# Performance work log

Hardware: AMD Instinct MI355X
Metric: run time of the kernel (lower is better)

The kernel has to match this reference:

```python
import jax, jax.numpy as jnp
import numpy as np

N = 50000   # total nodes
E = 600000  # total edges
F = 128     # in_features == hidden_features
H = 128
L = 4       # layers_count
B = 256     # number of graphs in batch
M = 200     # molecule_features
OUT = 12    # out_features
MH = H // 4 # molecular head width


def setup_inputs() -> dict:
    key = jax.random.key(0)
    ks = jax.random.split(key, 16)
    x = jax.random.normal(ks[0], (N, F), dtype=jnp.float32)
    edge_index = jax.random.randint(ks[1], (2, E), 0, N, dtype=jnp.int64)
    # sorted segment ids; guarantee every graph has >=1 node
    batch = jnp.sort(jnp.concatenate([
        jnp.arange(B, dtype=jnp.int64),
        jax.random.randint(ks[2], (N - B,), 0, B, dtype=jnp.int64)]))
    molecule_features = jax.random.normal(ks[3], (B, M), dtype=jnp.float32)
    s = 0.05
    Ws = jax.random.normal(ks[4], (L, H, H), dtype=jnp.float32) * s
    bs = jnp.zeros((L, H), dtype=jnp.float32)
    Wm = jax.random.normal(ks[5], (M, MH), dtype=jnp.float32) * s
    bm = jnp.zeros((MH,), dtype=jnp.float32)
    gamma = jnp.ones((MH,), dtype=jnp.float32)   # BatchNorm1d affine (eval mode, running stats 0/1)
    beta = jnp.zeros((MH,), dtype=jnp.float32)
    W1 = jax.random.normal(ks[6], (2 * H + MH, H), dtype=jnp.float32) * s  # mlp in = 288
    b1 = jnp.zeros((H,), dtype=jnp.float32)
    W2 = jax.random.normal(ks[7], (H, OUT), dtype=jnp.float32) * s
    b2 = jnp.zeros((OUT,), dtype=jnp.float32)
    return dict(x=x, edge_index=edge_index, batch=batch,
                molecule_features=molecule_features, Ws=Ws, bs=bs,
                Wm=Wm, bm=bm, gamma=gamma, beta=beta,
                W1=W1, b1=b1, W2=W2, b2=b2)


def gcn_conv(x, src, dst, W, b):
    # GCNConv: D^{-1/2} (A + I) D^{-1/2} X W + b, degrees include self loops
    ones = jnp.ones((E,), dtype=x.dtype)
    deg = jax.ops.segment_sum(ones, dst, num_segments=N) + 1.0  # self loop
    dis = jax.lax.rsqrt(deg)
    norm = dis[src] * dis[dst]                      # [E]
    xw = x @ W                                      # [N,H]
    msg = xw[src] * norm[:, None]                   # gather + scale
    agg = jax.ops.segment_sum(msg, dst, num_segments=N)
    agg = agg + xw * (dis * dis)[:, None]           # self-loop term
    return agg + b


def reference(x, edge_index, batch, molecule_features, Ws, bs, Wm, bm,
              gamma, beta, W1, b1, W2, b2):
    src, dst = edge_index[0], edge_index[1]
    h = x
    for l in range(L):
        y = jax.nn.relu(gcn_conv(h, src, dst, Ws[l], bs[l]))
        h = y + h  # residual (in == hidden); dropout is identity in eval
    max_pool = jax.ops.segment_max(h, batch, num_segments=B)
    add_pool = jax.ops.segment_sum(h, batch, num_segments=B)
    # molecular head: Linear -> Dropout(eval=identity) -> BatchNorm1d(eval) -> ReLU
    mol = molecule_features @ Wm + bm
    mol = jax.nn.relu(mol * gamma + beta)  # running_mean=0, running_var=1
    z = jnp.concatenate((max_pool, add_pool, mol), axis=1)  # [B, 288]
    z = jax.nn.relu(z @ W1 + b1)
    return z @ W2 + b2  # [B, OUT]
```

## Files before the change

### kernel.cpp

```cpp
#include <hip/hip_runtime.h>
#include <hip/hip_fp16.h>
#include <math.h>

static constexpr int NN  = 50000;
static constexpr int NE  = 600000;
static constexpr int HD  = 128;
static constexpr int NL  = 4;
static constexpr int NB  = 256;
static constexpr int NM  = 200;
static constexpr int NO  = 12;
static constexpr int NMH = 32;

#define MAX4(ac, b) { (ac).x = fmaxf((ac).x,(b).x); (ac).y = fmaxf((ac).y,(b).y); (ac).z = fmaxf((ac).z,(b).z); (ac).w = fmaxf((ac).w,(b).w); }
#define ADD4(ac, b) { (ac).x += (b).x; (ac).y += (b).y; (ac).z += (b).z; (ac).w += (b).w; }

typedef short bfx8 __attribute__((ext_vector_type(8)));
typedef float f32x4 __attribute__((ext_vector_type(4)));

__device__ __forceinline__ unsigned short f2bf(float f) {
  unsigned int u = __float_as_uint(f);
  unsigned int r = (u + 0x7fffu + ((u >> 16) & 1u)) >> 16;
  return (unsigned short)r;
}
__device__ __forceinline__ float bflo(unsigned int p) { return __uint_as_float(p << 16); }
__device__ __forceinline__ float bfhi(unsigned int p) { return __uint_as_float(p & 0xffff0000u); }
__device__ __forceinline__ float h2f_hi(unsigned e) {
  return __half2float(__ushort_as_half((unsigned short)(e >> 16)));
}

__global__ void k_hist(const int* __restrict__ dst, int* __restrict__ counts) {
  int e = blockIdx.x * blockDim.x + threadIdx.x;
  if (e < NE) atomicAdd(&counts[dst[e]], 1);
}

__global__ void k_scan1(const int* __restrict__ counts, int* __restrict__ incl,
                        int* __restrict__ bsum, float* __restrict__ dis) {
  __shared__ int s[256];
  int i = blockIdx.x * 256 + threadIdx.x;
  int v = (i < NN) ? counts[i] : 0;
  if (i < NN) dis[i] = rsqrtf((float)(v + 1));
  s[threadIdx.x] = v;
  __syncthreads();
  for (int off = 1; off < 256; off <<= 1) {
    int t = (threadIdx.x >= off) ? s[threadIdx.x - off] : 0;
    __syncthreads();
    s[threadIdx.x] += t;
    __syncthreads();
  }
  if (i < NN) incl[i] = s[threadIdx.x];
  if (threadIdx.x == 255) bsum[blockIdx.x] = s[255];
}

__global__ void k_scan2(const int* __restrict__ bsum, int* __restrict__ boff, int nblocks) {
  __shared__ int s[256];
  int v = (threadIdx.x < nblocks) ? bsum[threadIdx.x] : 0;
  s[threadIdx.x] = v;
  __syncthreads();
  for (int off = 1; off < 256; off <<= 1) {
    int t = (threadIdx.x >= off) ? s[threadIdx.x - off] : 0;
    __syncthreads();
    s[threadIdx.x] += t;
    __syncthreads();
  }
  boff[threadIdx.x] = s[threadIdx.x] - v;
}

__global__ void k_scan3(const int* __restrict__ counts, int* __restrict__ rowst, const int* __restrict__ boff) {
  int i = blockIdx.x * 256 + threadIdx.x;
  if (i < NN) {
    rowst[i] = rowst[i] - counts[i] + boff[blockIdx.x];
    if (i == NN - 1) rowst[NN] = NE;
  }
}

__global__ void k_fill(const int* __restrict__ src, const int* __restrict__ dst,
                       const int* __restrict__ rowst, const float* __restrict__ dis,
                       int* __restrict__ cur, unsigned* __restrict__ csr) {
  int e = blockIdx.x * blockDim.x + threadIdx.x;
  if (e < NE) {
    int d = dst[e];
    int s = src[e];
    int p = atomicAdd(&cur[d], 1);
    unsigned hb = (unsigned)__half_as_ushort(__float2half(dis[s]));
    csr[rowst[d] + p] = (hb << 16) | (unsigned)s;
  }
}

__global__ void k_goffs(const int* __restrict__ batch, int* __restrict__ goffs) {
  int i = blockIdx.x * blockDim.x + threadIdx.x;
  if (i >= NN) return;
  int b = batch[i];
  if (i == 0) {
    for (int g = 0; g <= b; ++g) goffs[g] = 0;
  } else {
    int pb = batch[i - 1];
    for (int g = pb + 1; g <= b; ++g) goffs[g] = i;
  }
  if (i == NN - 1) goffs[NB] = NN;
}

__global__ void k_tobf(const float4* __restrict__ in, ushort4* __restrict__ outb, int n4) {
  int i = blockIdx.x * blockDim.x + threadIdx.x;
  if (i < n4) {
    float4 v = in[i];
    outb[i] = make_ushort4(f2bf(v.x), f2bf(v.y), f2bf(v.z), f2bf(v.w));
  }
}

__global__ void k_wT(const float* __restrict__ Ws, unsigned short* __restrict__ wT) {
  int i = blockIdx.x * blockDim.x + threadIdx.x;
  if (i < NL * HD * HD) {
    int l = i >> 14, rem = i & 16383, n = rem >> 7, k = rem & 127;
    wT[i] = f2bf(Ws[l * 16384 + k * 128 + n]);
  }
}

__launch_bounds__(256)
__global__ void k_gemm_mfma(const unsigned short* __restrict__ A,
                            const unsigned short* __restrict__ WT,
                            unsigned short* __restrict__ C) {
  const int wave = threadIdx.x >> 6;
  const int lane = threadIdx.x & 63;
  const int m_base = blockIdx.x * 128 + wave * 32;
  const int lr = lane & 15;
  const int kg = lane >> 4;

  f32x4 acc[2][8];
#pragma unroll
  for (int mi = 0; mi < 2; ++mi)
#pragma unroll
    for (int nj = 0; nj < 8; ++nj) acc[mi][nj] = (f32x4){0.f, 0.f, 0.f, 0.f};

  int ra0 = m_base + lr;       if (ra0 > NN - 1) ra0 = NN - 1;
  int ra1 = m_base + 16 + lr;  if (ra1 > NN - 1) ra1 = NN - 1;

#pragma unroll
  for (int kb = 0; kb < 4; ++kb) {
    const int k0 = kb * 32 + kg * 8;
    bfx8 a0 = *(const bfx8*)&A[(size_t)ra0 * HD + k0];
    bfx8 a1 = *(const bfx8*)&A[(size_t)ra1 * HD + k0];
#pragma unroll
    for (int nj = 0; nj < 8; ++nj) {
      bfx8 b = *(const bfx8*)&WT[(nj * 16 + lr) * HD + k0];
      acc[0][nj] = __builtin_amdgcn_mfma_f32_16x16x32_bf16(a0, b, acc[0][nj], 0, 0, 0);
      acc[1][nj] = __builtin_amdgcn_mfma_f32_16x16x32_bf16(a1, b, acc[1][nj], 0, 0, 0);
    }
  }

  const int col = lane & 15;
  const int rbase = (lane >> 4) * 4;
#pragma unroll
  for (int mi = 0; mi < 2; ++mi) {
#pragma unroll
    for (int r = 0; r < 4; ++r) {
      int row = m_base + mi * 16 + rbase + r;
      if (row < NN) {
#pragma unroll
        for (int nj = 0; nj < 8; ++nj) {
          C[(size_t)row * HD + nj * 16 + col] = f2bf(acc[mi][nj][r]);
        }
      }
    }
  }
}

#define AGG_EDGE(e, p) { float nm = h2f_hi(e) * dn; \
    acc.x += nm * bflo((p).x); acc.y += nm * bfhi((p).x); \
    acc.z += nm * bflo((p).y); acc.w += nm * bfhi((p).y); }

__launch_bounds__(256)
__global__ void k_agg_h(const unsigned short* __restrict__ xw, const float* __restrict__ dis,
                        const int* __restrict__ rowst, const unsigned* __restrict__ csr,
                        const float* __restrict__ bias, const unsigned short* __restrict__ hinb,
                        unsigned short* __restrict__ houtb, int fh) {
  int slot = threadIdx.x >> 4;
  int lane = threadIdx.x & 15;
  int n = blockIdx.x * 16 + slot;
  if (n >= NN) return;

  const uint2* xwb = (const uint2*)xw;
  const int fo = fh * 16 + lane;

  float dn = dis[n];
  float4 acc;
  {
    uint2 p = xwb[(size_t)n * 32 + fo];
    float sl = dn * dn;
    acc.x = bflo(p.x) * sl; acc.y = bfhi(p.x) * sl;
    acc.z = bflo(p.y) * sl; acc.w = bfhi(p.y) * sl;
  }

  int s0 = rowst[n], s1 = rowst[n + 1];
  int idx = s0;
  for (; idx + 8 <= s1; idx += 8) {
    unsigned e0 = csr[idx],     e1 = csr[idx + 1], e2 = csr[idx + 2], e3 = csr[idx + 3];
    unsigned e4 = csr[idx + 4], e5 = csr[idx + 5], e6 = csr[idx + 6], e7 = csr[idx + 7];
    uint2 p0 = xwb[(size_t)(e0 & 0xffffu) * 32 + fo];
    uint2 p1 = xwb[(size_t)(e1 & 0xffffu) * 32 + fo];
    uint2 p2 = xwb[(size_t)(e2 & 0xffffu) * 32 + fo];
    uint2 p3 = xwb[(size_t)(e3 & 0xffffu) * 32 + fo];
    uint2 p4 = xwb[(size_t)(e4 & 0xffffu) * 32 + fo];
    uint2 p5 = xwb[(size_t)(e5 & 0xffffu) * 32 + fo];
    uint2 p6 = xwb[(size_t)(e6 & 0xffffu) * 32 + fo];
    uint2 p7 = xwb[(size_t)(e7 & 0xffffu) * 32 + fo];
    AGG_EDGE(e0, p0); AGG_EDGE(e1, p1); AGG_EDGE(e2, p2); AGG_EDGE(e3, p3);
    AGG_EDGE(e4, p4); AGG_EDGE(e5, p5); AGG_EDGE(e6, p6); AGG_EDGE(e7, p7);
  }
  for (; idx + 4 <= s1; idx += 4) {
    unsigned e0 = csr[idx], e1 = csr[idx + 1], e2 = csr[idx + 2], e3 = csr[idx + 3];
    uint2 p0 = xwb[(size_t)(e0 & 0xffffu) * 32 + fo];
    uint2 p1 = xwb[(size_t)(e1 & 0xffffu) * 32 + fo];
    uint2 p2 = xwb[(size_t)(e2 & 0xffffu) * 32 + fo];
    uint2 p3 = xwb[(size_t)(e3 & 0xffffu) * 32 + fo];
    AGG_EDGE(e0, p0); AGG_EDGE(e1, p1); AGG_EDGE(e2, p2); AGG_EDGE(e3, p3);
  }
  for (; idx < s1; ++idx) {
    unsigned e0 = csr[idx];
    uint2 p0 = xwb[(size_t)(e0 & 0xffffu) * 32 + fo];
    AGG_EDGE(e0, p0);
  }

  float4 b4 = *(const float4*)&bias[fh * 64 + lane * 4];
  uint2 hp = ((const uint2*)hinb)[(size_t)n * 32 + fo];
  float4 outv;
  outv.x = fmaxf(acc.x + b4.x, 0.f) + bflo(hp.x);
  outv.y = fmaxf(acc.y + b4.y, 0.f) + bfhi(hp.x);
  outv.z = fmaxf(acc.z + b4.z, 0.f) + bflo(hp.y);
  outv.w = fmaxf(acc.w + b4.w, 0.f) + bfhi(hp.y);
  ((ushort4*)houtb)[(size_t)n * 32 + fo] =
      make_ushort4(f2bf(outv.x), f2bf(outv.y), f2bf(outv.z), f2bf(outv.w));
}

__launch_bounds__(1024)
__global__ void k_pool(const unsigned short* __restrict__ hb, const int* __restrict__ goffs,
                       float* __restrict__ pooled) {
  __shared__ float4 smax[32][32];
  __shared__ float4 ssum[32][32];
  int g = blockIdx.x;
  int slot = threadIdx.x >> 5;
  int lane = threadIdx.x & 31;
  int a = goffs[g], bnd = goffs[g + 1];
  const uint2* hb2 = (const uint2*)hb;

  float4 mx = make_float4(-INFINITY, -INFINITY, -INFINITY, -INFINITY);
  float4 sm = make_float4(0.f, 0.f, 0.f, 0.f);
  for (int i = a + slot; i < bnd; i += 32) {
    uint2 p = hb2[(size_t)i * 32 + lane];
    float4 v = make_float4(bflo(p.x), bfhi(p.x), bflo(p.y), bfhi(p.y));
    MAX4(mx, v);
    ADD4(sm, v);
  }
  smax[slot][lane] = mx;
  ssum[slot][lane] = sm;
  __syncthreads();
#pragma unroll
  for (int off = 16; off >= 1; off >>= 1) {
    if (slot < off) {
      float4 m2 = smax[slot + off][lane];
      float4 s2 = ssum[slot + off][lane];
      float4 m1 = smax[slot][lane];
      float4 s1 = ssum[slot][lane];
      MAX4(m1, m2);
      ADD4(s1, s2);
      smax[slot][lane] = m1;
      ssum[slot][lane] = s1;
    }
    __syncthreads();
  }
  if (slot == 0) {
    *(float4*)&pooled[g * 256 + lane * 4]       = smax[0][lane];
    *(float4*)&pooled[g * 256 + 128 + lane * 4] = ssum[0][lane];
  }
}

__global__ void k_head(const float* __restrict__ pooled, const float* __restrict__ mf,
                       const float* __restrict__ Wm, const float* __restrict__ bm,
                       const float* __restrict__ gamma, const float* __restrict__ beta,
                       const float* __restrict__ W1, const float* __restrict__ b1,
                       const float* __restrict__ W2, const float* __restrict__ b2,
                       float* __restrict__ out) {
  __shared__ float z[288];
  __shared__ float z1[128];
  int g = blockIdx.x, t = threadIdx.x;
  z[t] = pooled[g * 256 + t];
  z[128 + t] = pooled[g * 256 + 128 + t];
  if (t < NMH) {
    float acc = bm[t];
    for (int k = 0; k < NM; ++k) acc += mf[g * NM + k] * Wm[k * NMH + t];
    acc = acc * gamma[t] + beta[t];
    z[256 + t] = fmaxf(acc, 0.f);
  }
  __syncthreads();
  float acc = b1[t];
  for (int k = 0; k < 288; ++k) acc += z[k] * W1[k * HD + t];
  z1[t] = fmaxf(acc, 0.f);
  __syncthreads();
  if (t < NO) {
    float a2 = b2[t];
    for (int k = 0; k < HD; ++k) a2 += z1[k] * W2[k * NO + t];
    out[g * NO + t] = a2;
  }
}

extern "C" void kernel_launch(void* const* d_in, const int* in_sizes, int n_in,
                              void* d_out, int out_size, void* d_ws, size_t ws_size,
                              hipStream_t stream) {
  const float* x     = (const float*)d_in[0];
  const int*   eidx  = (const int*)d_in[1];
  const int*   batch = (const int*)d_in[2];
  const float* mf    = (const float*)d_in[3];
  const float* Ws    = (const float*)d_in[4];
  const float* bs    = (const float*)d_in[5];
  const float* Wm    = (const float*)d_in[6];
  const float* bm    = (const float*)d_in[7];
  const float* gamma = (const float*)d_in[8];
  const float* beta  = (const float*)d_in[9];
  const float* W1    = (const float*)d_in[10];
  const float* b1    = (const float*)d_in[11];
  const float* W2    = (const float*)d_in[12];
  const float* b2    = (const float*)d_in[13];
  float* out = (float*)d_out;

  const int* src = eidx;
  const int* dst = eidx + NE;

  char* w = (char*)d_ws;
  size_t off = 0;
  auto alloc = [&](size_t bytes) -> void* {
    void* p = w + off;
    off += (bytes + 255) & ~(size_t)255;
    return p;
  };
  float* dis    = (float*)alloc((size_t)NN * 4);
  unsigned short* xw  = (unsigned short*)alloc((size_t)NN * HD * 2);
  unsigned short* xbf = (unsigned short*)alloc((size_t)NN * HD * 2);
  unsigned short* hbf = (unsigned short*)alloc((size_t)NN * HD * 2);
  unsigned short* wT  = (unsigned short*)alloc((size_t)NL * HD * HD * 2);
  int* counts   = (int*)alloc((size_t)NN * 4);
  int* cur      = (int*)alloc((size_t)NN * 4);
  int* rowst    = (int*)alloc((size_t)(NN + 1) * 4);
  unsigned* csr = (unsigned*)alloc((size_t)NE * 4);
  int* bsum     = (int*)alloc(256 * 4);
  int* boff     = (int*)alloc(256 * 4);
  int* goffs    = (int*)alloc((size_t)(NB + 1) * 4);
  float* pooled = (float*)alloc((size_t)NB * 256 * 4);
  (void)ws_size;

  const int SB = (NN + 255) / 256;

  hipMemsetAsync(counts, 0, (size_t)NN * 4, stream);
  hipMemsetAsync(cur, 0, (size_t)NN * 4, stream);

  k_hist<<<(NE + 255) / 256, 256, 0, stream>>>(dst, counts);
  k_scan1<<<SB, 256, 0, stream>>>(counts, rowst, bsum, dis);
  k_scan2<<<1, 256, 0, stream>>>(bsum, boff, SB);
  k_scan3<<<SB, 256, 0, stream>>>(counts, rowst, boff);
  k_fill<<<(NE + 255) / 256, 256, 0, stream>>>(src, dst, rowst, dis, cur, csr);

  k_goffs<<<SB, 256, 0, stream>>>(batch, goffs);
  k_tobf<<<((NN * HD / 4) + 255) / 256, 256, 0, stream>>>((const float4*)x, (ushort4*)xbf, NN * HD / 4);
  k_wT<<<(NL * HD * HD + 255) / 256, 256, 0, stream>>>(Ws, wT);

  const int AB = (NN + 15) / 16;
  for (int l = 0; l < NL; ++l) {
    const unsigned short* gin_bf = (l == 0) ? xbf : hbf;
    k_gemm_mfma<<<(NN + 127) / 128, 256, 0, stream>>>(gin_bf, wT + (size_t)l * HD * HD, xw);
    k_agg_h<<<AB, 256, 0, stream>>>(xw, dis, rowst, csr, bs + (size_t)l * HD, gin_bf, hbf, 0);
    k_agg_h<<<AB, 256, 0, stream>>>(xw, dis, rowst, csr, bs + (size_t)l * HD, gin_bf, hbf, 1);
  }

  k_pool<<<NB, 1024, 0, stream>>>(hbf, goffs, pooled);
  k_head<<<NB, 128, 0, stream>>>(pooled, mf, Wm, bm, gamma, beta, W1, b1, W2, b2, out);
}
```

Baseline: 302.7 us.

## Merge feature-half aggregation passes into one wide-load kernel and fuse setup kernels

The two per-layer aggregation launches, each covering one half of the features, become a single kernel. In it every lane gathers 16 bytes (8 bf16 features) per neighbour, so the CSR row is walked once instead of twice per layer. The bf16 conversion, weight transpose and graph-offset kernels are folded into one setup launch. The CSR fill now decrements the histogram counts instead of using a separate zeroed cursor array, which drops one memset and one buffer. In exchange, each thread holds more accumulator registers, and edge order within a row changes, which can slightly alter the float summation order.

```diff
diff --git a/kernel.cpp b/kernel.cpp
--- a/kernel.cpp
+++ b/kernel.cpp
@@ -75,43 +75,42 @@
 
 __global__ void k_fill(const int* __restrict__ src, const int* __restrict__ dst,
                        const int* __restrict__ rowst, const float* __restrict__ dis,
-                       int* __restrict__ cur, unsigned* __restrict__ csr) {
+                       int* __restrict__ counts, unsigned* __restrict__ csr) {
   int e = blockIdx.x * blockDim.x + threadIdx.x;
   if (e < NE) {
     int d = dst[e];
     int s = src[e];
-    int p = atomicAdd(&cur[d], 1);
+    int o = atomicSub(&counts[d], 1);
     unsigned hb = (unsigned)__half_as_ushort(__float2half(dis[s]));
-    csr[rowst[d] + p] = (hb << 16) | (unsigned)s;
-  }
-}
-
-__global__ void k_goffs(const int* __restrict__ batch, int* __restrict__ goffs) {
+    csr[rowst[d] + o - 1] = (hb << 16) | (unsigned)s;
+  }
+}
+
+static constexpr int NT_TOBF = NN * HD / 4;
+static constexpr int NT_WT   = NL * HD * HD;
+static constexpr int NT_ALL  = NT_TOBF + NT_WT + NN;
+
+__global__ void k_setup(const float4* __restrict__ x4, ushort4* __restrict__ xbf4,
+                        const float* __restrict__ Ws, unsigned short* __restrict__ wT,
+                        const int* __restrict__ batch, int* __restrict__ goffs) {
   int i = blockIdx.x * blockDim.x + threadIdx.x;
-  if (i >= NN) return;
-  int b = batch[i];
-  if (i == 0) {
-    for (int g = 0; g <= b; ++g) goffs[g] = 0;
-  } else {
-    int pb = batch[i - 1];
-    for (int g = pb + 1; g <= b; ++g) goffs[g] = i;
-  }
-  if (i == NN - 1) goffs[NB] = NN;
-}
-
-__global__ void k_tobf(const float4* __restrict__ in, ushort4* __restrict__ outb, int n4) {
-  int i = blockIdx.x * blockDim.x + threadIdx.x;
-  if (i < n4) {
-    float4 v = in[i];
-    outb[i] = make_ushort4(f2bf(v.x), f2bf(v.y), f2bf(v.z), f2bf(v.w));
-  }
-}
-
-__global__ void k_wT(const float* __restrict__ Ws, unsigned short* __restrict__ wT) {
-  int i = blockIdx.x * blockDim.x + threadIdx.x;
-  if (i < NL * HD * HD) {
-    int l = i >> 14, rem = i & 16383, n = rem >> 7, k = rem & 127;
-    wT[i] = f2bf(Ws[l * 16384 + k * 128 + n]);
+  if (i < NT_TOBF) {
+    float4 v = x4[i];
+    xbf4[i] = make_ushort4(f2bf(v.x), f2bf(v.y), f2bf(v.z), f2bf(v.w));
+  } else if (i < NT_TOBF + NT_WT) {
+    int j = i - NT_TOBF;
+    int l = j >> 14, rem = j & 16383, n = rem >> 7, k = rem & 127;
+    wT[j] = f2bf(Ws[l * 16384 + k * 128 + n]);
+  } else if (i < NT_ALL) {
+    int j = i - NT_TOBF - NT_WT;
+    int b = batch[j];
+    if (j == 0) {
+      for (int g = 0; g <= b; ++g) goffs[g] = 0;
+    } else {
+      int pb = batch[j - 1];
+      for (int g = pb + 1; g <= b; ++g) goffs[g] = j;
+    }
+    if (j == NN - 1) goffs[NB] = NN;
   }
 }
 
@@ -164,30 +163,33 @@
   }
 }
 
-#define AGG_EDGE(e, p) { float nm = h2f_hi(e) * dn; \
-    acc.x += nm * bflo((p).x); acc.y += nm * bfhi((p).x); \
-    acc.z += nm * bflo((p).y); acc.w += nm * bfhi((p).y); }
+#define AGGE(e, p) { float nm = h2f_hi(e) * dn; \
+    acc[0] += nm * bflo((p).x); acc[1] += nm * bfhi((p).x); \
+    acc[2] += nm * bflo((p).y); acc[3] += nm * bfhi((p).y); \
+    acc[4] += nm * bflo((p).z); acc[5] += nm * bfhi((p).z); \
+    acc[6] += nm * bflo((p).w); acc[7] += nm * bfhi((p).w); }
 
 __launch_bounds__(256)
-__global__ void k_agg_h(const unsigned short* __restrict__ xw, const float* __restrict__ dis,
+__global__ void k_agg16(const unsigned short* __restrict__ xw, const float* __restrict__ dis,
                         const int* __restrict__ rowst, const unsigned* __restrict__ csr,
                         const float* __restrict__ bias, const unsigned short* __restrict__ hinb,
-                        unsigned short* __restrict__ houtb, int fh) {
+                        unsigned short* __restrict__ houtb) {
   int slot = threadIdx.x >> 4;
   int lane = threadIdx.x & 15;
   int n = blockIdx.x * 16 + slot;
   if (n >= NN) return;
 
-  const uint2* xwb = (const uint2*)xw;
-  const int fo = fh * 16 + lane;
+  const uint4* xw4 = (const uint4*)xw;
 
   float dn = dis[n];
-  float4 acc;
+  float acc[8];
   {
-    uint2 p = xwb[(size_t)n * 32 + fo];
+    uint4 p = xw4[(size_t)n * 16 + lane];
     float sl = dn * dn;
-    acc.x = bflo(p.x) * sl; acc.y = bfhi(p.x) * sl;
-    acc.z = bflo(p.y) * sl; acc.w = bfhi(p.y) * sl;
+    acc[0] = bflo(p.x) * sl; acc[1] = bfhi(p.x) * sl;
+    acc[2] = bflo(p.y) * sl; acc[3] = bfhi(p.y) * sl;
+    acc[4] = bflo(p.z) * sl; acc[5] = bfhi(p.z) * sl;
+    acc[6] = bflo(p.w) * sl; acc[7] = bfhi(p.w) * sl;
   }
 
   int s0 = rowst[n], s1 = rowst[n + 1];
@@ -195,40 +197,48 @@
   for (; idx + 8 <= s1; idx += 8) {
     unsigned e0 = csr[idx],     e1 = csr[idx + 1], e2 = csr[idx + 2], e3 = csr[idx + 3];
     unsigned e4 = csr[idx + 4], e5 = csr[idx + 5], e6 = csr[idx + 6], e7 = csr[idx + 7];
-    uint2 p0 = xwb[(size_t)(e0 & 0xffffu) * 32 + fo];
-    uint2 p1 = xwb[(size_t)(e1 & 0xffffu) * 32 + fo];
-    uint2 p2 = xwb[(size_t)(e2 & 0xffffu) * 32 + fo];
-    uint2 p3 = xwb[(size_t)(e3 & 0xffffu) * 32 + fo];
-    uint2 p4 = xwb[(size_t)(e4 & 0xffffu) * 32 + fo];
-    uint2 p5 = xwb[(size_t)(e5 & 0xffffu) * 32 + fo];
-    uint2 p6 = xwb[(size_t)(e6 & 0xffffu) * 32 + fo];
-    uint2 p7 = xwb[(size_t)(e7 & 0xffffu) * 32 + fo];
-    AGG_EDGE(e0, p0); AGG_EDGE(e1, p1); AGG_EDGE(e2, p2); AGG_EDGE(e3, p3);
-    AGG_EDGE(e4, p4); AGG_EDGE(e5, p5); AGG_EDGE(e6, p6); AGG_EDGE(e7, p7);
+    uint4 p0 = xw4[(size_t)(e0 & 0xffffu) * 16 + lane];
+    uint4 p1 = xw4[(size_t)(e1 & 0xffffu) * 16 + lane];
+    uint4 p2 = xw4[(size_t)(e2 & 0xffffu) * 16 + lane];
+    uint4 p3 = xw4[(size_t)(e3 & 0xffffu) * 16 + lane];
+    uint4 p4 = xw4[(size_t)(e4 & 0xffffu) * 16 + lane];
+    uint4 p5 = xw4[(size_t)(e5 & 0xffffu) * 16 + lane];
+    uint4 p6 = xw4[(size_t)(e6 & 0xffffu) * 16 + lane];
+    uint4 p7 = xw4[(size_t)(e7 & 0xffffu) * 16 + lane];
+    AGGE(e0, p0); AGGE(e1, p1); AGGE(e2, p2); AGGE(e3, p3);
+    AGGE(e4, p4); AGGE(e5, p5); AGGE(e6, p6); AGGE(e7, p7);
   }
   for (; idx + 4 <= s1; idx += 4) {
     unsigned e0 = csr[idx], e1 = csr[idx + 1], e2 = csr[idx + 2], e3 = csr[idx + 3];
-    uint2 p0 = xwb[(size_t)(e0 & 0xffffu) * 32 + fo];
-    uint2 p1 = xwb[(size_t)(e1 & 0xffffu) * 32 + fo];
-    uint2 p2 = xwb[(size_t)(e2 & 0xffffu) * 32 + fo];
-    uint2 p3 = xwb[(size_t)(e3 & 0xffffu) * 32 + fo];
-    AGG_EDGE(e0, p0); AGG_EDGE(e1, p1); AGG_EDGE(e2, p2); AGG_EDGE(e3, p3);
+    uint4 p0 = xw4[(size_t)(e0 & 0xffffu) * 16 + lane];
+    uint4 p1 = xw4[(size_t)(e1 & 0xffffu) * 16 + lane];
+    uint4 p2 = xw4[(size_t)(e2 & 0xffffu) * 16 + lane];
+    uint4 p3 = xw4[(size_t)(e3 & 0xffffu) * 16 + lane];
+    AGGE(e0, p0); AGGE(e1, p1); AGGE(e2, p2); AGGE(e3, p3);
   }
   for (; idx < s1; ++idx) {
     unsigned e0 = csr[idx];
-    uint2 p0 = xwb[(size_t)(e0 & 0xffffu) * 32 + fo];
-    AGG_EDGE(e0, p0);
-  }
-
-  float4 b4 = *(const float4*)&bias[fh * 64 + lane * 4];
-  uint2 hp = ((const uint2*)hinb)[(size_t)n * 32 + fo];
-  float4 outv;
-  outv.x = fmaxf(acc.x + b4.x, 0.f) + bflo(hp.x);
-  outv.y = fmaxf(acc.y + b4.y, 0.f) + bfhi(hp.x);
-  outv.z = fmaxf(acc.z + b4.z, 0.f) + bflo(hp.y);
-  outv.w = fmaxf(acc.w + b4.w, 0.f) + bfhi(hp.y);
-  ((ushort4*)houtb)[(size_t)n * 32 + fo] =
-      make_ushort4(f2bf(outv.x), f2bf(outv.y), f2bf(outv.z), f2bf(outv.w));
+    uint4 p0 = xw4[(size_t)(e0 & 0xffffu) * 16 + lane];
+    AGGE(e0, p0);
+  }
+
+  float4 ba = *(const float4*)&bias[lane * 8];
+  float4 bb = *(const float4*)&bias[lane * 8 + 4];
+  uint4 hp = ((const uint4*)hinb)[(size_t)n * 16 + lane];
+  float o0 = fmaxf(acc[0] + ba.x, 0.f) + bflo(hp.x);
+  float o1 = fmaxf(acc[1] + ba.y, 0.f) + bfhi(hp.x);
+  float o2 = fmaxf(acc[2] + ba.z, 0.f) + bflo(hp.y);
+  float o3 = fmaxf(acc[3] + ba.w, 0.f) + bfhi(hp.y);
+  float o4 = fmaxf(acc[4] + bb.x, 0.f) + bflo(hp.z);
+  float o5 = fmaxf(acc[5] + bb.y, 0.f) + bfhi(hp.z);
+  float o6 = fmaxf(acc[6] + bb.z, 0.f) + bflo(hp.w);
+  float o7 = fmaxf(acc[7] + bb.w, 0.f) + bfhi(hp.w);
+  uint4 ov;
+  ov.x = (unsigned)f2bf(o0) | ((unsigned)f2bf(o1) << 16);
+  ov.y = (unsigned)f2bf(o2) | ((unsigned)f2bf(o3) << 16);
+  ov.z = (unsigned)f2bf(o4) | ((unsigned)f2bf(o5) << 16);
+  ov.w = (unsigned)f2bf(o6) | ((unsigned)f2bf(o7) << 16);
+  ((uint4*)houtb)[(size_t)n * 16 + lane] = ov;
 }
 
 __launch_bounds__(1024)
@@ -337,7 +347,6 @@
   unsigned short* hbf = (unsigned short*)alloc((size_t)NN * HD * 2);
   unsigned short* wT  = (unsigned short*)alloc((size_t)NL * HD * HD * 2);
   int* counts   = (int*)alloc((size_t)NN * 4);
-  int* cur      = (int*)alloc((size_t)NN * 4);
   int* rowst    = (int*)alloc((size_t)(NN + 1) * 4);
   unsigned* csr = (unsigned*)alloc((size_t)NE * 4);
   int* bsum     = (int*)alloc(256 * 4);
@@ -349,24 +358,20 @@
   const int SB = (NN + 255) / 256;
 
   hipMemsetAsync(counts, 0, (size_t)NN * 4, stream);
-  hipMemsetAsync(cur, 0, (size_t)NN * 4, stream);
 
   k_hist<<<(NE + 255) / 256, 256, 0, stream>>>(dst, counts);
   k_scan1<<<SB, 256, 0, stream>>>(counts, rowst, bsum, dis);
   k_scan2<<<1, 256, 0, stream>>>(bsum, boff, SB);
   k_scan3<<<SB, 256, 0, stream>>>(counts, rowst, boff);
-  k_fill<<<(NE + 255) / 256, 256, 0, stream>>>(src, dst, rowst, dis, cur, csr);
-
-  k_goffs<<<SB, 256, 0, stream>>>(batch, goffs);
-  k_tobf<<<((NN * HD / 4) + 255) / 256, 256, 0, stream>>>((const float4*)x, (ushort4*)xbf, NN * HD / 4);
-  k_wT<<<(NL * HD * HD + 255) / 256, 256, 0, stream>>>(Ws, wT);
-
-  const int AB = (NN + 15) / 16;
+  k_fill<<<(NE + 255) / 256, 256, 0, stream>>>(src, dst, rowst, dis, counts, csr);
+
+  k_setup<<<(NT_ALL + 255) / 256, 256, 0, stream>>>((const float4*)x, (ushort4*)xbf,
+                                                    Ws, wT, batch, goffs);
+
   for (int l = 0; l < NL; ++l) {
     const unsigned short* gin_bf = (l == 0) ? xbf : hbf;
     k_gemm_mfma<<<(NN + 127) / 128, 256, 0, stream>>>(gin_bf, wT + (size_t)l * HD * HD, xw);
-    k_agg_h<<<AB, 256, 0, stream>>>(xw, dis, rowst, csr, bs + (size_t)l * HD, gin_bf, hbf, 0);
-    k_agg_h<<<AB, 256, 0, stream>>>(xw, dis, rowst, csr, bs + (size_t)l * HD, gin_bf, hbf, 1);
+    k_agg16<<<(NN + 15) / 16, 256, 0, stream>>>(xw, dis, rowst, csr, bs + (size_t)l * HD, gin_bf, hbf);
   }
 
   k_pool<<<NB, 1024, 0, stream>>>(hbf, goffs, pooled);
```

Measured after the change: 276.9 us. 1.09x faster.
